# Kernel optimization log

Measured on AMD Instinct MI355X. Metric: run time of the kernel, lower is better.

## Reference

```python
import jax, jax.numpy as jnp
import numpy as np

H = 64  # hidden size, hard-coded in the module

def _lstm_layer(x, W_ih, W_hh, b_ih, b_hh):
    """One LSTM layer, batch_first. x: [B, T, D_in] -> [B, T, H].
    PyTorch gate order: i, f, g, o. Zero initial state (module passes None)."""
    B = x.shape[0]
    # precompute input projection for all timesteps (the parallelizable part)
    xp = jnp.einsum('btd,gd->btg', x, W_ih) + b_ih + b_hh  # [B, T, 4H]
    xp = jnp.swapaxes(xp, 0, 1)                            # [T, B, 4H] for scan
    h0 = jnp.zeros((B, H), x.dtype)
    c0 = jnp.zeros((B, H), x.dtype)

    def step(carry, xt):
        h, c = carry
        gates = xt + h @ W_hh.T                            # [B, 4H]
        i, f, g, o = jnp.split(gates, 4, axis=-1)
        i = jax.nn.sigmoid(i)
        f = jax.nn.sigmoid(f)
        g = jnp.tanh(g)
        o = jax.nn.sigmoid(o)
        c = f * c + i * g
        h = o * jnp.tanh(c)
        return (h, c), h

    _, hs = jax.lax.scan(step, (h0, c0), xp)               # hs: [T, B, H]
    return jnp.swapaxes(hs, 0, 1)                          # [B, T, H]


def setup_inputs() -> dict:
    B, T, I = 256, 512, 128
    key = jax.random.key(0)
    ks = jax.random.split(key, 16)
    s = 0.1  # weight scale ~ torch default init range, avoids gate saturation
    inp = {
        'x': jax.random.normal(ks[0], (B, T, I), jnp.float32),
        'W_ih0': jax.random.normal(ks[1], (4 * H, I), jnp.float32) * s,
        'W_hh0': jax.random.normal(ks[2], (4 * H, H), jnp.float32) * s,
        'b_ih0': jax.random.normal(ks[3], (4 * H,), jnp.float32) * s,
        'b_hh0': jax.random.normal(ks[4], (4 * H,), jnp.float32) * s,
        'W_ih1': jax.random.normal(ks[5], (4 * H, H), jnp.float32) * s,
        'W_hh1': jax.random.normal(ks[6], (4 * H, H), jnp.float32) * s,
        'b_ih1': jax.random.normal(ks[7], (4 * H,), jnp.float32) * s,
        'b_hh1': jax.random.normal(ks[8], (4 * H,), jnp.float32) * s,
        'W_ih2': jax.random.normal(ks[9], (4 * H, H), jnp.float32) * s,
        'W_hh2': jax.random.normal(ks[10], (4 * H, H), jnp.float32) * s,
        'b_ih2': jax.random.normal(ks[11], (4 * H,), jnp.float32) * s,
        'b_hh2': jax.random.normal(ks[12], (4 * H,), jnp.float32) * s,
        'W_out': jax.random.normal(ks[13], (2, H), jnp.float32) * s,
        'b_out': jax.random.normal(ks[14], (2,), jnp.float32) * s,
    }
    return inp


def reference(x, W_ih0, W_hh0, b_ih0, b_hh0,
              W_ih1, W_hh1, b_ih1, b_hh1,
              W_ih2, W_hh2, b_ih2, b_hh2,
              W_out, b_out):
    h = _lstm_layer(x, W_ih0, W_hh0, b_ih0, b_hh0)
    h = _lstm_layer(h, W_ih1, W_hh1, b_ih1, b_hh1)
    h = _lstm_layer(h, W_ih2, W_hh2, b_ih2, b_hh2)
    # final linear on last timestep: r_out[:, -1, :] @ W_out.T + b_out
    return h[:, -1, :] @ W_out.T + b_out  # [B, 2]
```

## Files before the change

### kernel.cpp

```cpp
#include <hip/hip_runtime.h>
#include <cstddef>
#include <cstdint>

#define NB 256
#define NT 512
#define H4 256

typedef _Float16 v2h __attribute__((ext_vector_type(2)));
typedef int v4i __attribute__((ext_vector_type(4)));
typedef int v2i __attribute__((ext_vector_type(2)));

__device__ __forceinline__ float dpp_xor1(float x) {
    int r = __builtin_amdgcn_update_dpp(0, __float_as_int(x), 0xB1, 0xF, 0xF, true);
    return __int_as_float(r);
}
__device__ __forceinline__ float dpp_xor2(float x) {
    int r = __builtin_amdgcn_update_dpp(0, __float_as_int(x), 0x4E, 0xF, 0xF, true);
    return __int_as_float(r);
}
__device__ __forceinline__ float sel4(float x0, float x1, float x2, float x3, int m) {
    float lo = (m & 1) ? x1 : x0;
    float hi = (m & 1) ? x3 : x2;
    return (m & 2) ? hi : lo;
}
__device__ __forceinline__ int pack2h(float a, float b) {
    v2h p; p.x = (_Float16)a; p.y = (_Float16)b;
    return __builtin_bit_cast(int, p);
}
#if __has_builtin(__builtin_amdgcn_fdot2)
__device__ __forceinline__ float dot2acc(int wb, int xb, float c) {
    return __builtin_amdgcn_fdot2(__builtin_bit_cast(v2h, wb),
                                  __builtin_bit_cast(v2h, xb), c, false);
}
#else
__device__ __forceinline__ float dot2acc(int wb, int xb, float c) {
    v2h w = __builtin_bit_cast(v2h, wb);
    v2h x = __builtin_bit_cast(v2h, xb);
    c = __builtin_fmaf((float)w.x, (float)x.x, c);
    c = __builtin_fmaf((float)w.y, (float)x.y, c);
    return c;
}
#endif

__device__ __forceinline__ void mv4(const int wq[4][8], const int hh[8], float p[4]) {
    #pragma unroll
    for (int j = 0; j < 4; ++j) {
        float a0 = 0.f, a1 = 0.f;
        #pragma unroll
        for (int q = 0; q < 8; q += 2) {
            a0 = dot2acc(wq[j][q], hh[q], a0);
            a1 = dot2acc(wq[j][q + 1], hh[q + 1], a1);
        }
        p[j] = a0 + a1;
    }
}
__device__ __forceinline__ void mv4acc(const int wq[4][8], const int hh[8], float p[4]) {
    #pragma unroll
    for (int j = 0; j < 4; ++j) {
        float a0 = 0.f, a1 = 0.f;
        #pragma unroll
        for (int q = 0; q < 8; q += 2) {
            a0 = dot2acc(wq[j][q], hh[q], a0);
            a1 = dot2acc(wq[j][q + 1], hh[q + 1], a1);
        }
        p[j] += a0 + a1;
    }
}

__global__ void pack_w(const float* __restrict__ W, int* __restrict__ out) {
    int idx = blockIdx.x * 256 + threadIdx.x;
    int lane = idx >> 5;
    int jq = idx & 31;
    int j = jq >> 3, q = jq & 7;
    int ks = lane & 3, u = lane >> 2;
    const float* Wr = W + (size_t)(((ks ^ j) * 64) + u) * 64 + ks * 16 + 2 * q;
    out[idx] = pack2h(Wr[0], Wr[1]);
}

__global__ void transpose_w(const float* __restrict__ W, float* __restrict__ Wt, int K) {
    int idx = blockIdx.x * 256 + threadIdx.x;
    if (idx < 256 * K) {
        int n = idx / K, k = idx - n * K;
        Wt[k * 256 + n] = W[idx];
    }
}

template <int K>
__global__ __launch_bounds__(256) void gemm_xp(
    const float* __restrict__ X, const float* __restrict__ Wt,
    const float* __restrict__ b1, const float* __restrict__ b2,
    _Float16* __restrict__ XPh)
{
    constexpr int TM = 64;
    constexpr int KC = 16;
    __shared__ __align__(16) float xT[K][TM + 4];
    __shared__ __align__(16) float wc[KC][256];
    const int m0 = blockIdx.x * TM;
    const int t  = threadIdx.x;
    const int cg = (t & 63) * 4;
    const int rg = (t >> 6) * 16;

    for (int idx = t; idx < TM * K; idx += 256) {
        int r = idx / K, k = idx - r * K;
        xT[k][r] = X[(size_t)(m0 + r) * K + k];
    }

    float acc[16][4];
    #pragma unroll
    for (int i = 0; i < 16; ++i)
        #pragma unroll
        for (int j = 0; j < 4; ++j) acc[i][j] = 0.f;

    for (int kc = 0; kc < K; kc += KC) {
        __syncthreads();
        #pragma unroll
        for (int i = 0; i < 4; ++i) {
            int e4 = (t + i * 256) * 4;
            int k = e4 >> 8, n = e4 & 255;
            *(float4*)&wc[k][n] = *(const float4*)&Wt[(size_t)(kc + k) * 256 + n];
        }
        __syncthreads();
        #pragma unroll
        for (int k = 0; k < KC; ++k) {
            float4 w = *(const float4*)&wc[k][cg];
            float xr[16];
            #pragma unroll
            for (int q = 0; q < 4; ++q)
                *(float4*)&xr[q * 4] = *(const float4*)&xT[kc + k][rg + q * 4];
            #pragma unroll
            for (int rr = 0; rr < 16; ++rr) {
                acc[rr][0] += xr[rr] * w.x;
                acc[rr][1] += xr[rr] * w.y;
                acc[rr][2] += xr[rr] * w.z;
                acc[rr][3] += xr[rr] * w.w;
            }
        }
    }

    float bias[4];
    #pragma unroll
    for (int j = 0; j < 4; ++j) bias[j] = b1[cg + j] + b2[cg + j];
    #pragma unroll
    for (int rr = 0; rr < 16; ++rr) {
        v2i o;
        o.x = pack2h(acc[rr][0] + bias[0], acc[rr][1] + bias[1]);
        o.y = pack2h(acc[rr][2] + bias[2], acc[rr][3] + bias[3]);
        *(v2i*)&XPh[(size_t)(m0 + rg + rr) * 256 + cg] = o;
    }
}

__global__ __attribute__((amdgpu_flat_work_group_size(768, 768)))
__attribute__((amdgpu_waves_per_eu(3, 3)))
void lstm_fused3(
    const _Float16* __restrict__ xp,
    const int* __restrict__ WP,
    const float* __restrict__ bi1, const float* __restrict__ bh1,
    const float* __restrict__ bi2, const float* __restrict__ bh2,
    float* __restrict__ hl)
{
    const int tid = threadIdx.x;
    const int b = blockIdx.x;
    const int L = tid >> 8;
    const int t256 = tid & 255;
    const int ks = t256 & 3;
    const int u = t256 >> 2;

    __shared__ __align__(16) char lds_force[90112];
    _Float16 (*hb)[2][64] = (_Float16 (*)[2][64])lds_force;

    const int Lu = __builtin_amdgcn_readfirstlane(L);

    const int mh = (Lu == 0) ? 0 : (Lu == 1) ? 1 : 3;
    int wgb[4][8];
    {
        const v4i* wp = (const v4i*)(WP + (size_t)mh * 8192 + t256 * 32);
        #pragma unroll
        for (int cch = 0; cch < 8; ++cch) {
            v4i v = wp[cch];
            int j = cch >> 1, q0 = (cch & 1) * 4;
            wgb[j][q0 + 0] = v.x; wgb[j][q0 + 1] = v.y;
            wgb[j][q0 + 2] = v.z; wgb[j][q0 + 3] = v.w;
        }
    }
    int wib[4][8];
    float bsum = 0.f;
    if (Lu > 0) {
        const int mi = (Lu == 1) ? 2 : 4;
        const v4i* wp = (const v4i*)(WP + (size_t)mi * 8192 + t256 * 32);
        #pragma unroll
        for (int cch = 0; cch < 8; ++cch) {
            v4i v = wp[cch];
            int j = cch >> 1, q0 = (cch & 1) * 4;
            wib[j][q0 + 0] = v.x; wib[j][q0 + 1] = v.y;
            wib[j][q0 + 2] = v.z; wib[j][q0 + 3] = v.w;
        }
        const float* bi = (Lu == 1) ? bi1 : bi2;
        const float* bh = (Lu == 1) ? bh1 : bh2;
        bsum = bi[ks * 64 + u] + bh[ks * 64 + u];
    }

    const float LOG2E = 1.4426950408889634f;
    const float nM  = (ks == 2) ? (-2.f * LOG2E) : -LOG2E;
    const float A   = (ks == 2) ? 2.f : 1.f;
    const float Bc  = (ks == 2) ? -1.f : 0.f;
    const float nMt = -2.f * LOG2E;

    if (tid < 192) ((int*)lds_force)[tid] = 0;

    const v4i* pOwn0 = (const v4i*)&hb[Lu][0][ks * 16];
    const v4i* pOwn1 = (const v4i*)&hb[Lu][1][ks * 16];
    const int Lin = (Lu > 0) ? (Lu - 1) : 0;
    const v4i* pIn0 = (const v4i*)&hb[Lin][0][ks * 16];
    const v4i* pIn1 = (const v4i*)&hb[Lin][1][ks * 16];
    _Float16* pW0 = &hb[Lu][0][u];
    _Float16* pW1 = &hb[Lu][1][u];

    const _Float16* xpb = xp + (size_t)b * NT * H4 + (ks * 64 + u);
    float xr[4];
    if (Lu == 0) {
        #pragma unroll
        for (int d = 0; d < 4; ++d) xr[d] = (float)xpb[(size_t)d * H4];
    }

    asm volatile("s_waitcnt lgkmcnt(0)" ::: "memory");
    __builtin_amdgcn_s_barrier();
    __builtin_amdgcn_sched_barrier(0);

    float c = 0.f, h = 0.f;
    const bool writer = (ks == 0);

#define BAR() do { asm volatile("s_waitcnt lgkmcnt(0)" ::: "memory"); \
                   __builtin_amdgcn_s_barrier(); \
                   __builtin_amdgcn_sched_barrier(0); } while (0)

#define LD8(dst, ptr) do { v4i t0_ = (ptr)[0]; v4i t1_ = (ptr)[1]; \
    dst[0] = t0_.x; dst[1] = t0_.y; dst[2] = t0_.z; dst[3] = t0_.w; \
    dst[4] = t1_.x; dst[5] = t1_.y; dst[6] = t1_.z; dst[7] = t1_.w; } while (0)

#define RED(S, p) float S = p[0] + dpp_xor1(p[1]); \
    S += dpp_xor2(p[2]) + dpp_xor2(dpp_xor1(p[3]))

#define ACT_CELL(pre) do { \
    float e_ = __builtin_amdgcn_exp2f((pre) * nM); \
    float y_ = __builtin_amdgcn_rcpf(1.f + e_); \
    float act_ = __builtin_fmaf(A, y_, Bc); \
    float a1_ = dpp_xor1(act_), a2_ = dpp_xor2(act_), a3_ = dpp_xor2(a1_); \
    float ig_ = (ks & 1) ? (a1_ * a3_) : (act_ * a2_); \
    float fv_ = sel4(a1_, act_, a3_, a2_, ks); \
    float ov_ = sel4(a3_, a2_, a1_, act_, ks); \
    c = __builtin_fmaf(fv_, c, ig_); \
    float e2_ = __builtin_amdgcn_exp2f(c * nMt); \
    float y2_ = __builtin_amdgcn_rcpf(1.f + e2_); \
    h = ov_ * __builtin_fmaf(2.f, y2_, -1.f); \
} while (0)

#define STEP0(D) do { int s_ = s4 + (D); if (s_ < NT) { \
    int hh[8]; LD8(hh, (((D) & 1) ? pOwn1 : pOwn0)); \
    float p[4]; mv4(wgb, hh, p); \
    float xc = xr[(D)]; \
    int tn_ = s_ + 4; if (tn_ > NT - 1) tn_ = NT - 1; \
    xr[(D)] = (float)xpb[(size_t)tn_ * H4]; \
    RED(S_, p); float pre_ = S_ + xc; \
    ACT_CELL(pre_); \
    if (writer) *((((D) + 1) & 1) ? pW1 : pW0) = (_Float16)h; \
} } while (0)

#define STEP1(D) do { int t_ = s4 + (D) - 1; if ((unsigned)t_ < NT) { \
    int hh[8]; LD8(hh, ((((D) + 1) & 1) ? pOwn1 : pOwn0)); \
    float p[4]; mv4(wgb, hh, p); \
    int gg[8]; LD8(gg, (((D) & 1) ? pIn1 : pIn0)); \
    mv4acc(wib, gg, p); \
    RED(S_, p); float pre_ = S_ + bsum; \
    ACT_CELL(pre_); \
    if (writer) *(((D) & 1) ? pW1 : pW0) = (_Float16)h; \
} } while (0)

#define STEP2(D) do { int t_ = s4 + (D) - 2; if ((unsigned)t_ < NT) { \
    int hh[8]; LD8(hh, (((D) & 1) ? pOwn1 : pOwn0)); \
    float p[4]; mv4(wgb, hh, p); \
    int gg[8]; LD8(gg, ((((D) + 1) & 1) ? pIn1 : pIn0)); \
    mv4acc(wib, gg, p); \
    RED(S_, p); float pre_ = S_ + bsum; \
    ACT_CELL(pre_); \
    if (writer) { \
        *((((D) + 1) & 1) ? pW1 : pW0) = (_Float16)h; \
        if (t_ == NT - 1) hl[(size_t)b * 64 + u] = h; \
    } \
} } while (0)

    for (int s4 = 0; s4 < NT + 4; s4 += 4) {
        if (Lu == 0) {
            STEP0(0); BAR(); STEP0(1); BAR(); STEP0(2); BAR(); STEP0(3); BAR();
        } else if (Lu == 1) {
            STEP1(0); BAR(); STEP1(1); BAR(); STEP1(2); BAR(); STEP1(3); BAR();
        } else {
            STEP2(0); BAR(); STEP2(1); BAR(); STEP2(2); BAR(); STEP2(3); BAR();
        }
    }
#undef STEP0
#undef STEP1
#undef STEP2
#undef ACT_CELL
#undef RED
#undef LD8
#undef BAR
}

__global__ __launch_bounds__(256) void final_linear(
    const float* __restrict__ hlv, const float* __restrict__ Wout,
    const float* __restrict__ bout, float* __restrict__ out)
{
    __shared__ float w[128];
    int t = threadIdx.x;
    if (t < 128) w[t] = Wout[t];
    __syncthreads();
    const float* h = hlv + (size_t)t * 64;
    float a0 = bout[0], a1 = bout[1];
    #pragma unroll 8
    for (int j = 0; j < 64; ++j) {
        float hv = h[j];
        a0 += hv * w[j];
        a1 += hv * w[64 + j];
    }
    out[t * 2 + 0] = a0;
    out[t * 2 + 1] = a1;
}

extern "C" void kernel_launch(void* const* d_in, const int* in_sizes, int n_in,
                              void* d_out, int out_size, void* d_ws, size_t ws_size,
                              hipStream_t stream)
{
    const float* x     = (const float*)d_in[0];
    const float* W_ih0 = (const float*)d_in[1];
    const float* W_hh0 = (const float*)d_in[2];
    const float* b_ih0 = (const float*)d_in[3];
    const float* b_hh0 = (const float*)d_in[4];
    const float* W_ih1 = (const float*)d_in[5];
    const float* W_hh1 = (const float*)d_in[6];
    const float* b_ih1 = (const float*)d_in[7];
    const float* b_hh1 = (const float*)d_in[8];
    const float* W_ih2 = (const float*)d_in[9];
    const float* W_hh2 = (const float*)d_in[10];
    const float* b_ih2 = (const float*)d_in[11];
    const float* b_hh2 = (const float*)d_in[12];
    const float* W_out = (const float*)d_in[13];
    const float* b_out = (const float*)d_in[14];
    float* out = (float*)d_out;

    const size_t M = (size_t)NB * NT;
    const size_t XP_BYTES  = M * H4 * sizeof(_Float16);
    const size_t WT0_BYTES = 128 * 256 * sizeof(float);
    const size_t WP_BYTES  = 5 * 8192 * sizeof(int);
    const size_t HL_BYTES  = NB * 64 * sizeof(float);
    if (ws_size < XP_BYTES + WT0_BYTES + WP_BYTES + HL_BYTES)
        return;

    char* ws = (char*)d_ws;
    _Float16* XPh = (_Float16*)ws;
    float* WT0 = (float*)(ws + XP_BYTES);
    int*   WP  = (int*)(ws + XP_BYTES + WT0_BYTES);
    float* HL  = (float*)(ws + XP_BYTES + WT0_BYTES + WP_BYTES);

    pack_w<<<32, 256, 0, stream>>>(W_hh0, WP + 0 * 8192);
    pack_w<<<32, 256, 0, stream>>>(W_hh1, WP + 1 * 8192);
    pack_w<<<32, 256, 0, stream>>>(W_ih1, WP + 2 * 8192);
    pack_w<<<32, 256, 0, stream>>>(W_hh2, WP + 3 * 8192);
    pack_w<<<32, 256, 0, stream>>>(W_ih2, WP + 4 * 8192);

    transpose_w<<<128, 256, 0, stream>>>(W_ih0, WT0, 128);
    gemm_xp<128><<<(int)(M / 64), 256, 0, stream>>>(x, WT0, b_ih0, b_hh0, XPh);

    lstm_fused3<<<NB, 768, 0, stream>>>(XPh, WP, b_ih1, b_hh1, b_ih2, b_hh2, HL);

    final_linear<<<1, 256, 0, stream>>>(HL, W_out, b_out, out);
}
```

Before: 472.2 us.

## Store input projection in fp32 and peel recurrence loop to drop per-step guards

The input-projection buffer changes from fp16 to fp32. This removes the pack and convert work in the GEMM and the fp16-to-float conversion in the layer-0 step, but doubles the bytes written and read. The recurrent loop is split into a guarded prologue, an unguarded steady-state body, and a guarded epilogue. The steady-state body drops the bounds checks, the clamped index math and the final-output check, and uses a pointer-bumped prefetch of the next projection value. The cost is a larger kernel and roughly double the traffic for the projection buffer.

```diff
diff --git a/kernel.cpp b/kernel.cpp
--- a/kernel.cpp
+++ b/kernel.cpp
@@ -8,7 +8,6 @@
 
 typedef _Float16 v2h __attribute__((ext_vector_type(2)));
 typedef int v4i __attribute__((ext_vector_type(4)));
-typedef int v2i __attribute__((ext_vector_type(2)));
 
 __device__ __forceinline__ float dpp_xor1(float x) {
     int r = __builtin_amdgcn_update_dpp(0, __float_as_int(x), 0xB1, 0xF, 0xF, true);
@@ -89,7 +88,7 @@
 __global__ __launch_bounds__(256) void gemm_xp(
     const float* __restrict__ X, const float* __restrict__ Wt,
     const float* __restrict__ b1, const float* __restrict__ b2,
-    _Float16* __restrict__ XPh)
+    float* __restrict__ XP)
 {
     constexpr int TM = 64;
     constexpr int KC = 16;
@@ -142,17 +141,19 @@
     for (int j = 0; j < 4; ++j) bias[j] = b1[cg + j] + b2[cg + j];
     #pragma unroll
     for (int rr = 0; rr < 16; ++rr) {
-        v2i o;
-        o.x = pack2h(acc[rr][0] + bias[0], acc[rr][1] + bias[1]);
-        o.y = pack2h(acc[rr][2] + bias[2], acc[rr][3] + bias[3]);
-        *(v2i*)&XPh[(size_t)(m0 + rg + rr) * 256 + cg] = o;
+        float4 o;
+        o.x = acc[rr][0] + bias[0];
+        o.y = acc[rr][1] + bias[1];
+        o.z = acc[rr][2] + bias[2];
+        o.w = acc[rr][3] + bias[3];
+        *(float4*)&XP[(size_t)(m0 + rg + rr) * 256 + cg] = o;
     }
 }
 
 __global__ __attribute__((amdgpu_flat_work_group_size(768, 768)))
 __attribute__((amdgpu_waves_per_eu(3, 3)))
 void lstm_fused3(
-    const _Float16* __restrict__ xp,
+    const float* __restrict__ xp,
     const int* __restrict__ WP,
     const float* __restrict__ bi1, const float* __restrict__ bh1,
     const float* __restrict__ bi2, const float* __restrict__ bh2,
@@ -214,12 +215,13 @@
     const v4i* pIn1 = (const v4i*)&hb[Lin][1][ks * 16];
     _Float16* pW0 = &hb[Lu][0][u];
     _Float16* pW1 = &hb[Lu][1][u];
-
-    const _Float16* xpb = xp + (size_t)b * NT * H4 + (ks * 64 + u);
+    float* hlp = hl + (size_t)b * 64 + u;
+
+    const float* xpb = xp + (size_t)b * NT * H4 + (ks * 64 + u);
     float xr[4];
     if (Lu == 0) {
         #pragma unroll
-        for (int d = 0; d < 4; ++d) xr[d] = (float)xpb[(size_t)d * H4];
+        for (int d = 0; d < 4; ++d) xr[d] = xpb[(size_t)d * H4];
     }
 
     asm volatile("s_waitcnt lgkmcnt(0)" ::: "memory");
@@ -254,18 +256,18 @@
     h = ov_ * __builtin_fmaf(2.f, y2_, -1.f); \
 } while (0)
 
-#define STEP0(D) do { int s_ = s4 + (D); if (s_ < NT) { \
+#define CSTEP0(D) do { int s_ = s4 + (D); if (s_ < NT) { \
     int hh[8]; LD8(hh, (((D) & 1) ? pOwn1 : pOwn0)); \
     float p[4]; mv4(wgb, hh, p); \
     float xc = xr[(D)]; \
     int tn_ = s_ + 4; if (tn_ > NT - 1) tn_ = NT - 1; \
-    xr[(D)] = (float)xpb[(size_t)tn_ * H4]; \
+    xr[(D)] = xpb[(size_t)tn_ * H4]; \
     RED(S_, p); float pre_ = S_ + xc; \
     ACT_CELL(pre_); \
     if (writer) *((((D) + 1) & 1) ? pW1 : pW0) = (_Float16)h; \
 } } while (0)
 
-#define STEP1(D) do { int t_ = s4 + (D) - 1; if ((unsigned)t_ < NT) { \
+#define CSTEP1(D) do { int t_ = s4 + (D) - 1; if ((unsigned)t_ < NT) { \
     int hh[8]; LD8(hh, ((((D) + 1) & 1) ? pOwn1 : pOwn0)); \
     float p[4]; mv4(wgb, hh, p); \
     int gg[8]; LD8(gg, (((D) & 1) ? pIn1 : pIn0)); \
@@ -275,7 +277,7 @@
     if (writer) *(((D) & 1) ? pW1 : pW0) = (_Float16)h; \
 } } while (0)
 
-#define STEP2(D) do { int t_ = s4 + (D) - 2; if ((unsigned)t_ < NT) { \
+#define CSTEP2(D) do { int t_ = s4 + (D) - 2; if ((unsigned)t_ < NT) { \
     int hh[8]; LD8(hh, (((D) & 1) ? pOwn1 : pOwn0)); \
     float p[4]; mv4(wgb, hh, p); \
     int gg[8]; LD8(gg, ((((D) + 1) & 1) ? pIn1 : pIn0)); \
@@ -284,22 +286,81 @@
     ACT_CELL(pre_); \
     if (writer) { \
         *((((D) + 1) & 1) ? pW1 : pW0) = (_Float16)h; \
-        if (t_ == NT - 1) hl[(size_t)b * 64 + u] = h; \
+        if (t_ == NT - 1) *hlp = h; \
     } \
 } } while (0)
 
-    for (int s4 = 0; s4 < NT + 4; s4 += 4) {
+#define FSTEP0(D) do { \
+    int hh[8]; LD8(hh, (((D) & 1) ? pOwn1 : pOwn0)); \
+    float p[4]; mv4(wgb, hh, p); \
+    float xc = xr[(D)]; \
+    xr[(D)] = *xnext; xnext += H4; \
+    RED(S_, p); float pre_ = S_ + xc; \
+    ACT_CELL(pre_); \
+    if (writer) *((((D) + 1) & 1) ? pW1 : pW0) = (_Float16)h; \
+} while (0)
+
+#define FSTEP1(D) do { \
+    int hh[8]; LD8(hh, ((((D) + 1) & 1) ? pOwn1 : pOwn0)); \
+    float p[4]; mv4(wgb, hh, p); \
+    int gg[8]; LD8(gg, (((D) & 1) ? pIn1 : pIn0)); \
+    mv4acc(wib, gg, p); \
+    RED(S_, p); float pre_ = S_ + bsum; \
+    ACT_CELL(pre_); \
+    if (writer) *(((D) & 1) ? pW1 : pW0) = (_Float16)h; \
+} while (0)
+
+#define FSTEP2(D) do { \
+    int hh[8]; LD8(hh, (((D) & 1) ? pOwn1 : pOwn0)); \
+    float p[4]; mv4(wgb, hh, p); \
+    int gg[8]; LD8(gg, ((((D) + 1) & 1) ? pIn1 : pIn0)); \
+    mv4acc(wib, gg, p); \
+    RED(S_, p); float pre_ = S_ + bsum; \
+    ACT_CELL(pre_); \
+    if (writer) *((((D) + 1) & 1) ? pW1 : pW0) = (_Float16)h; \
+} while (0)
+
+    {
+        int s4 = 0;
         if (Lu == 0) {
-            STEP0(0); BAR(); STEP0(1); BAR(); STEP0(2); BAR(); STEP0(3); BAR();
+            CSTEP0(0); BAR(); CSTEP0(1); BAR(); CSTEP0(2); BAR(); CSTEP0(3); BAR();
         } else if (Lu == 1) {
-            STEP1(0); BAR(); STEP1(1); BAR(); STEP1(2); BAR(); STEP1(3); BAR();
+            CSTEP1(0); BAR(); CSTEP1(1); BAR(); CSTEP1(2); BAR(); CSTEP1(3); BAR();
         } else {
-            STEP2(0); BAR(); STEP2(1); BAR(); STEP2(2); BAR(); STEP2(3); BAR();
-        }
-    }
-#undef STEP0
-#undef STEP1
-#undef STEP2
+            CSTEP2(0); BAR(); CSTEP2(1); BAR(); CSTEP2(2); BAR(); CSTEP2(3); BAR();
+        }
+    }
+
+    const float* xnext = xpb + (size_t)8 * H4;
+    if (Lu == 0) {
+        for (int s4 = 4; s4 <= NT - 8; s4 += 4) {
+            FSTEP0(0); BAR(); FSTEP0(1); BAR(); FSTEP0(2); BAR(); FSTEP0(3); BAR();
+        }
+    } else if (Lu == 1) {
+        for (int s4 = 4; s4 <= NT - 8; s4 += 4) {
+            FSTEP1(0); BAR(); FSTEP1(1); BAR(); FSTEP1(2); BAR(); FSTEP1(3); BAR();
+        }
+    } else {
+        for (int s4 = 4; s4 <= NT - 8; s4 += 4) {
+            FSTEP2(0); BAR(); FSTEP2(1); BAR(); FSTEP2(2); BAR(); FSTEP2(3); BAR();
+        }
+    }
+
+    for (int s4 = NT - 4; s4 <= NT; s4 += 4) {
+        if (Lu == 0) {
+            CSTEP0(0); BAR(); CSTEP0(1); BAR(); CSTEP0(2); BAR(); CSTEP0(3); BAR();
+        } else if (Lu == 1) {
+            CSTEP1(0); BAR(); CSTEP1(1); BAR(); CSTEP1(2); BAR(); CSTEP1(3); BAR();
+        } else {
+            CSTEP2(0); BAR(); CSTEP2(1); BAR(); CSTEP2(2); BAR(); CSTEP2(3); BAR();
+        }
+    }
+#undef CSTEP0
+#undef CSTEP1
+#undef CSTEP2
+#undef FSTEP0
+#undef FSTEP1
+#undef FSTEP2
 #undef ACT_CELL
 #undef RED
 #undef LD8
@@ -348,7 +409,7 @@
     float* out = (float*)d_out;
 
     const size_t M = (size_t)NB * NT;
-    const size_t XP_BYTES  = M * H4 * sizeof(_Float16);
+    const size_t XP_BYTES  = M * H4 * sizeof(float);
     const size_t WT0_BYTES = 128 * 256 * sizeof(float);
     const size_t WP_BYTES  = 5 * 8192 * sizeof(int);
     const size_t HL_BYTES  = NB * 64 * sizeof(float);
@@ -356,7 +417,7 @@
         return;
 
     char* ws = (char*)d_ws;
-    _Float16* XPh = (_Float16*)ws;
+    float* XP  = (float*)ws;
     float* WT0 = (float*)(ws + XP_BYTES);
     int*   WP  = (int*)(ws + XP_BYTES + WT0_BYTES);
     float* HL  = (float*)(ws + XP_BYTES + WT0_BYTES + WP_BYTES);
@@ -368,9 +429,9 @@
     pack_w<<<32, 256, 0, stream>>>(W_ih2, WP + 4 * 8192);
 
     transpose_w<<<128, 256, 0, stream>>>(W_ih0, WT0, 128);
-    gemm_xp<128><<<(int)(M / 64), 256, 0, stream>>>(x, WT0, b_ih0, b_hh0, XPh);
-
-    lstm_fused3<<<NB, 768, 0, stream>>>(XPh, WP, b_ih1, b_hh1, b_ih2, b_hh2, HL);
+    gemm_xp<128><<<(int)(M / 64), 256, 0, stream>>>(x, WT0, b_ih0, b_hh0, XP);
+
+    lstm_fused3<<<NB, 768, 0, stream>>>(XP, WP, b_ih1, b_hh1, b_ih2, b_hh2, HL);
 
     final_linear<<<1, 256, 0, stream>>>(HL, W_out, b_out, out);
 }
```

Measured after the change: 480.6 us. No clear change (+1.8%).
